# Kernel optimization log

Measured on AMD Instinct MI355X. Metric: run time of the kernel, lower is better.

## Reference

```python
import jax, jax.numpy as jnp
import numpy as np

B, L, D, H = 4, 2048, 1024, 16
HD = D // H  # head_dim = 64


def setup_inputs() -> dict:
    key = jax.random.key(0)
    k1, k2, k3, k4 = jax.random.split(key, 4)
    x = jax.random.normal(k1, (B, L, D), dtype=jnp.float32)
    key_padding_mask = jax.random.randint(k2, (B, L), 0, 2) == 1
    scale = 1.0 / np.sqrt(D)
    Wqkv = jax.random.normal(k3, (3 * D, D), dtype=jnp.float32) * scale
    Wproj = jax.random.normal(k4, (D, D), dtype=jnp.float32) * scale
    return {"x": x, "key_padding_mask": key_padding_mask, "Wqkv": Wqkv, "Wproj": Wproj}


def reference(x, key_padding_mask, Wqkv, Wproj):
    b, l, d = x.shape
    qkv = jnp.einsum('bld,ed->ble', x, Wqkv)          # [B, L, 3D]
    q, k, v = jnp.split(qkv, 3, axis=-1)
    # [B, H, L, HD]
    q = q.reshape(b, l, H, HD).transpose(0, 2, 1, 3)
    k = k.reshape(b, l, H, HD).transpose(0, 2, 1, 3)
    v = v.reshape(b, l, H, HD).transpose(0, 2, 1, 3)
    scale = 1.0 / jnp.sqrt(jnp.asarray(HD, dtype=x.dtype))
    scores = jnp.einsum('bhqd,bhkd->bhqk', q, k) * scale  # [B, H, L, L]
    # key_padding_mask True = PAD -> -inf bias on key axis
    bias = jnp.where(key_padding_mask[:, None, None, :], -jnp.inf, 0.0).astype(x.dtype)
    attn = jax.nn.softmax(scores + bias, axis=-1)
    y = jnp.einsum('bhqk,bhkd->bhqd', attn, v)            # [B, H, L, HD]
    y = y.transpose(0, 2, 1, 3).reshape(b, l, d)          # [B, L, D]
    return jnp.einsum('bld,ed->ble', y, Wproj)
```

## Files before the change

### kernel.cpp

```cpp
#include <hip/hip_runtime.h>

#define L_SEQ 2048
#define DIM   1024
#define NH    16
#define HDIM  64
#define KDIM  1024

typedef short  short8 __attribute__((ext_vector_type(8)));
typedef __bf16 bf16x8 __attribute__((ext_vector_type(8)));
typedef __bf16 bf16x4 __attribute__((ext_vector_type(4)));
typedef float  f32x4  __attribute__((ext_vector_type(4)));
typedef unsigned u32x4 __attribute__((ext_vector_type(4)));

__device__ __forceinline__ unsigned short f2bf(float f) {
  unsigned u = __builtin_bit_cast(unsigned, f);
  u += 0x7fffu + ((u >> 16) & 1u);
  return (unsigned short)(u >> 16);
}

__device__ __forceinline__ void gload16(const void* g, void* l) {
  __builtin_amdgcn_global_load_lds(
      (const __attribute__((address_space(1))) void*)g,
      (__attribute__((address_space(3))) void*)l, 16, 0, 0);
}

__device__ __forceinline__ unsigned cvtpk(float a, float b) {
  unsigned r;
  asm("v_cvt_pk_bf16_f32 %0, %1, %2" : "=v"(r) : "v"(a), "v"(b));
  return r;
}
__device__ __forceinline__ void xchg(unsigned &a, unsigned &b) {
  asm("v_permlane32_swap_b32 %0, %1" : "+v"(a), "+v"(b));
  asm("v_permlane16_swap_b32 %0, %1" : "+v"(a), "+v"(b));
}

__global__ __launch_bounds__(256) void cvt_bf16(const float* __restrict__ src,
                                                unsigned short* __restrict__ dst,
                                                int n) {
  int i = (blockIdx.x * 256 + threadIdx.x) * 8;
  if (i >= n) return;
  f32x4 a = *(const f32x4*)(src + i);
  f32x4 b = *(const f32x4*)(src + i + 4);
  short8 o;
  o[0] = (short)f2bf(a[0]); o[1] = (short)f2bf(a[1]);
  o[2] = (short)f2bf(a[2]); o[3] = (short)f2bf(a[3]);
  o[4] = (short)f2bf(b[0]); o[5] = (short)f2bf(b[1]);
  o[6] = (short)f2bf(b[2]); o[7] = (short)f2bf(b[3]);
  *(short8*)(dst + i) = o;
}

__global__ __launch_bounds__(256) void zero_buf(f32x4* __restrict__ dst, int n4) {
  int i = blockIdx.x * 256 + threadIdx.x;
  if (i < n4) dst[i] = f32x4{0.f, 0.f, 0.f, 0.f};
}

__global__ __launch_bounds__(256) void mask_scan(const int* __restrict__ mask,
                                                 int* __restrict__ idx,
                                                 int* __restrict__ lc) {
  const int b = blockIdx.x, t = threadIdx.x;
  __shared__ int wsum[4];
  const int* mrow = mask + b * L_SEQ + t * 8;
  int m[8], c = 0;
#pragma unroll
  for (int i = 0; i < 8; ++i) { m[i] = mrow[i]; c += (m[i] == 0); }
  const int lane = t & 63, w = t >> 6;
  int sc = c;
#pragma unroll
  for (int d = 1; d < 64; d <<= 1) {
    int v = __shfl_up(sc, d);
    if (lane >= d) sc += v;
  }
  if (lane == 63) wsum[w] = sc;
  __syncthreads();
  int pre = sc - c;
  for (int i = 0; i < w; ++i) pre += wsum[i];
  int run = pre;
#pragma unroll
  for (int i = 0; i < 8; ++i) {
    idx[b * L_SEQ + t * 8 + i] = m[i] ? -1 : run;
    run += (m[i] == 0);
  }
  if (t == 255) lc[b] = run;
}

__device__ __forceinline__ void gemm128_mainloop(
    const unsigned short* __restrict__ A, const unsigned short* __restrict__ Bt,
    int m0, int n0, unsigned short* As, unsigned short* Bs, f32x4 (&acc)[4][4]) {
  const int t = threadIdx.x;
  const int wid = t >> 6, lane = t & 63;
  const int wm = wid >> 1, wn = wid & 1;
  const int lr = lane & 15, lk = (lane >> 4) * 8;
  for (int kt = 0; kt < KDIM / 64; ++kt) {
    __syncthreads();
#pragma unroll
    for (int i = 0; i < 4; ++i) {
      int c = i * 256 + t;
      int row = c >> 3, cc = (c & 7) * 8;
      gload16(A  + (size_t)(m0 + row) * KDIM + kt * 64 + cc, As + c * 8);
      gload16(Bt + (size_t)(n0 + row) * KDIM + kt * 64 + cc, Bs + c * 8);
    }
    asm volatile("s_waitcnt vmcnt(0)" ::: "memory");
    __syncthreads();
    bf16x8 af[4][2], bfv[4][2];
#pragma unroll
    for (int mf = 0; mf < 4; ++mf)
#pragma unroll
      for (int kh = 0; kh < 2; ++kh)
        af[mf][kh] = __builtin_bit_cast(bf16x8,
            *(const short8*)(As + (wm * 64 + mf * 16 + lr) * 64 + kh * 32 + lk));
#pragma unroll
    for (int nf = 0; nf < 4; ++nf)
#pragma unroll
      for (int kh = 0; kh < 2; ++kh)
        bfv[nf][kh] = __builtin_bit_cast(bf16x8,
            *(const short8*)(Bs + (wn * 64 + nf * 16 + lr) * 64 + kh * 32 + lk));
#pragma unroll
    for (int mf = 0; mf < 4; ++mf)
#pragma unroll
      for (int nf = 0; nf < 4; ++nf)
#pragma unroll
        for (int kh = 0; kh < 2; ++kh)
          acc[mf][nf] = __builtin_amdgcn_mfma_f32_16x16x32_bf16(
              af[mf][kh], bfv[nf][kh], acc[mf][nf], 0, 0, 0);
  }
}

__global__ __launch_bounds__(256) void gemm_qkv(
    const unsigned short* __restrict__ xb, const unsigned short* __restrict__ wb,
    const int* __restrict__ idx,
    unsigned short* __restrict__ qw, unsigned short* __restrict__ kw,
    unsigned short* __restrict__ vtw) {
  __shared__ unsigned short As[128 * 64], Bs[128 * 64];
  f32x4 acc[4][4] = {};
  const int n0 = blockIdx.x * 128, m0 = blockIdx.y * 128;
  gemm128_mainloop(xb, wb, m0, n0, As, Bs, acc);
  const int t = threadIdx.x, wid = t >> 6, lane = t & 63;
  const int wm = wid >> 1, wn = wid & 1;
  const int sec = n0 >> 10;
  const int nb = n0 & 1023;
  if (sec == 0) {
#pragma unroll
    for (int mf = 0; mf < 4; ++mf)
#pragma unroll
      for (int nf = 0; nf < 4; ++nf) {
        int e = nb + wn * 64 + nf * 16 + (lane & 15);
        int h = e >> 6, hd = e & 63;
#pragma unroll
        for (int r = 0; r < 4; ++r) {
          int m = m0 + wm * 64 + mf * 16 + (lane >> 4) * 4 + r;
          int b = m >> 11, li = m & 2047;
          qw[(((size_t)(b * NH + h)) * L_SEQ + li) * HDIM + hd] =
              f2bf(acc[mf][nf][r]);
        }
      }
  } else {
#pragma unroll
    for (int mf = 0; mf < 4; ++mf)
#pragma unroll
      for (int r = 0; r < 4; ++r) {
        int m = m0 + wm * 64 + mf * 16 + (lane >> 4) * 4 + r;
        int b = m >> 11, li = m & 2047;
        int tgt = idx[b * L_SEQ + li];
        if (tgt < 0) continue;
        size_t bb = (size_t)b * NH;
#pragma unroll
        for (int nf = 0; nf < 4; ++nf) {
          int e = nb + wn * 64 + nf * 16 + (lane & 15);
          int h = e >> 6, hd = e & 63;
          unsigned short val = f2bf(acc[mf][nf][r]);
          if (sec == 1) kw[((bb + h) * L_SEQ + tgt) * HDIM + hd] = val;
          else          vtw[((bb + h) * HDIM + hd) * L_SEQ + tgt] = val;
        }
      }
  }
}

__global__ __launch_bounds__(256) void gemm_proj(
    const unsigned short* __restrict__ yb, const unsigned short* __restrict__ wb,
    float* __restrict__ out) {
  __shared__ unsigned short As[128 * 64], Bs[128 * 64];
  f32x4 acc[4][4] = {};
  const int n0 = blockIdx.x * 128, m0 = blockIdx.y * 128;
  gemm128_mainloop(yb, wb, m0, n0, As, Bs, acc);
  const int t = threadIdx.x, wid = t >> 6, lane = t & 63;
  const int wm = wid >> 1, wn = wid & 1;
#pragma unroll
  for (int mf = 0; mf < 4; ++mf)
#pragma unroll
    for (int nf = 0; nf < 4; ++nf) {
      int e = n0 + wn * 64 + nf * 16 + (lane & 15);
#pragma unroll
      for (int r = 0; r < 4; ++r) {
        int m = m0 + wm * 64 + mf * 16 + (lane >> 4) * 4 + r;
        out[(size_t)m * DIM + e] = acc[mf][nf][r];
      }
    }
}

__global__ __launch_bounds__(256, 4) void attn_kernel(
    const unsigned short* __restrict__ qw, const unsigned short* __restrict__ kw,
    const unsigned short* __restrict__ vtw, const int* __restrict__ lc,
    unsigned short* __restrict__ yb) {
  __shared__ unsigned short Ks[2][64 * 64];
  __shared__ unsigned short Vts[2][64 * 64];
  const int bh = blockIdx.y;
  const int q0 = blockIdx.x * 128;
  const int b = bh >> 4, h = bh & 15;
  const int t = threadIdx.x, wid = t >> 6, lane = t & 63;
  const int lr = lane & 15, lk = (lane >> 4) * 8, g4 = (lane >> 4) * 4;
  const int swr = (lr & 7) << 3;
  const float KE = 0.18033688011112042f;

  const int Lcv = lc[b];
  const int nt = (Lcv + 63) >> 6;

  bf16x8 qf[2][2];
  const size_t qbase = (size_t)bh * L_SEQ + q0 + wid * 32;
#pragma unroll
  for (int qi = 0; qi < 2; ++qi)
#pragma unroll
    for (int kh = 0; kh < 2; ++kh)
      qf[qi][kh] = __builtin_bit_cast(bf16x8,
          *(const short8*)(qw + (qbase + qi * 16 + lr) * HDIM + kh * 32 + lk));

  f32x4 o[2][4] = {};
  float mrun[2] = {-3.0e38f, -3.0e38f};
  float lrun[2] = {0.f, 0.f};

  auto stage = [&](int buf, int kt) {
#pragma unroll
    for (int i = 0; i < 2; ++i) {
      int c = i * 256 + t;
      int row = c >> 3;
      int cs = ((c & 7) ^ (row & 7)) * 8;
      gload16(kw  + ((size_t)bh * L_SEQ + kt * 64 + row) * HDIM + cs, &Ks[buf][c * 8]);
      gload16(vtw + ((size_t)bh * HDIM + row) * L_SEQ + kt * 64 + cs, &Vts[buf][c * 8]);
    }
  };

  stage(0, 0);
  int cur = 0;

  for (int kt = 0; kt < nt; ++kt) {
    if (kt + 1 < nt) {
      stage(cur ^ 1, kt + 1);
      asm volatile("s_waitcnt vmcnt(4)" ::: "memory");
    } else {
      asm volatile("s_waitcnt vmcnt(0)" ::: "memory");
    }
    __builtin_amdgcn_s_barrier();
    __builtin_amdgcn_sched_barrier(0);

    const unsigned short* Kc = Ks[cur];
    f32x4 s[2][4] = {};
    __builtin_amdgcn_s_setprio(1);
#pragma unroll
    for (int nf = 0; nf < 4; ++nf) {
      bf16x8 k0 = __builtin_bit_cast(bf16x8,
          *(const short8*)(Kc + (nf * 16 + lr) * 64 + ((0 + lk) ^ swr)));
      bf16x8 k1 = __builtin_bit_cast(bf16x8,
          *(const short8*)(Kc + (nf * 16 + lr) * 64 + ((32 + lk) ^ swr)));
      s[0][nf] = __builtin_amdgcn_mfma_f32_16x16x32_bf16(k0, qf[0][0], s[0][nf], 0, 0, 0);
      s[0][nf] = __builtin_amdgcn_mfma_f32_16x16x32_bf16(k1, qf[0][1], s[0][nf], 0, 0, 0);
      s[1][nf] = __builtin_amdgcn_mfma_f32_16x16x32_bf16(k0, qf[1][0], s[1][nf], 0, 0, 0);
      s[1][nf] = __builtin_amdgcn_mfma_f32_16x16x32_bf16(k1, qf[1][1], s[1][nf], 0, 0, 0);
    }
    __builtin_amdgcn_s_setprio(0);

    if (kt == nt - 1) {
      int kbase = kt * 64 + g4;
#pragma unroll
      for (int nf = 0; nf < 4; ++nf)
#pragma unroll
        for (int r = 0; r < 4; ++r)
          if (kbase + nf * 16 + r >= Lcv) {
            s[0][nf][r] = -3.0e38f;
            s[1][nf][r] = -3.0e38f;
          }
    }

    float pmax[2];
#pragma unroll
    for (int qi = 0; qi < 2; ++qi) {
      float a0 = fmaxf(fmaxf(s[qi][0][0], s[qi][0][1]), fmaxf(s[qi][0][2], s[qi][0][3]));
      float a1 = fmaxf(fmaxf(s[qi][1][0], s[qi][1][1]), fmaxf(s[qi][1][2], s[qi][1][3]));
      float a2 = fmaxf(fmaxf(s[qi][2][0], s[qi][2][1]), fmaxf(s[qi][2][2], s[qi][2][3]));
      float a3 = fmaxf(fmaxf(s[qi][3][0], s[qi][3][1]), fmaxf(s[qi][3][2], s[qi][3][3]));
      float mm = fmaxf(fmaxf(a0, a1), fmaxf(a2, a3));
      mm = fmaxf(mm, __shfl_xor(mm, 16));
      mm = fmaxf(mm, __shfl_xor(mm, 32));
      pmax[qi] = mm;
    }

    bool need = (pmax[0] > mrun[0] + 8.0f) || (pmax[1] > mrun[1] + 8.0f);
    if (__any(need)) {
#pragma unroll
      for (int qi = 0; qi < 2; ++qi) {
        float mn = fmaxf(mrun[qi], pmax[qi]);
        float al = __builtin_amdgcn_exp2f((mrun[qi] - mn) * KE);
        mrun[qi] = mn;
        lrun[qi] *= al;
#pragma unroll
        for (int df = 0; df < 4; ++df) o[qi][df] *= al;
      }
    }

    bf16x8 pb[2][2];
#pragma unroll
    for (int qi = 0; qi < 2; ++qi) {
      float mk_ = mrun[qi] * KE;
      f32x4 rs4 = {0.f, 0.f, 0.f, 0.f};
#pragma unroll
      for (int nf = 0; nf < 4; ++nf) {
#pragma unroll
        for (int r = 0; r < 4; ++r)
          s[qi][nf][r] = __builtin_amdgcn_exp2f(s[qi][nf][r] * KE - mk_);
        rs4 += s[qi][nf];
      }
      float rsum = (rs4[0] + rs4[1]) + (rs4[2] + rs4[3]);
      rsum += __shfl_xor(rsum, 16);
      rsum += __shfl_xor(rsum, 32);
      lrun[qi] += rsum;
      unsigned w00 = cvtpk(s[qi][0][0], s[qi][0][1]);
      unsigned w01 = cvtpk(s[qi][0][2], s[qi][0][3]);
      unsigned w10 = cvtpk(s[qi][1][0], s[qi][1][1]);
      unsigned w11 = cvtpk(s[qi][1][2], s[qi][1][3]);
      unsigned w20 = cvtpk(s[qi][2][0], s[qi][2][1]);
      unsigned w21 = cvtpk(s[qi][2][2], s[qi][2][3]);
      unsigned w30 = cvtpk(s[qi][3][0], s[qi][3][1]);
      unsigned w31 = cvtpk(s[qi][3][2], s[qi][3][3]);
      xchg(w00, w10);
      xchg(w01, w11);
      xchg(w20, w30);
      xchg(w21, w31);
      u32x4 f0 = {w00, w01, w10, w11};
      u32x4 f1 = {w20, w21, w30, w31};
      pb[qi][0] = __builtin_bit_cast(bf16x8, f0);
      pb[qi][1] = __builtin_bit_cast(bf16x8, f1);
    }

    const unsigned short* Vc = Vts[cur];
    __builtin_amdgcn_s_setprio(1);
#pragma unroll
    for (int df = 0; df < 4; ++df) {
      bf16x8 v0 = __builtin_bit_cast(bf16x8,
          *(const short8*)(Vc + (df * 16 + lr) * 64 + ((0 + lk) ^ swr)));
      bf16x8 v1 = __builtin_bit_cast(bf16x8,
          *(const short8*)(Vc + (df * 16 + lr) * 64 + ((32 + lk) ^ swr)));
      o[0][df] = __builtin_amdgcn_mfma_f32_16x16x32_bf16(v0, pb[0][0], o[0][df], 0, 0, 0);
      o[0][df] = __builtin_amdgcn_mfma_f32_16x16x32_bf16(v1, pb[0][1], o[0][df], 0, 0, 0);
      o[1][df] = __builtin_amdgcn_mfma_f32_16x16x32_bf16(v0, pb[1][0], o[1][df], 0, 0, 0);
      o[1][df] = __builtin_amdgcn_mfma_f32_16x16x32_bf16(v1, pb[1][1], o[1][df], 0, 0, 0);
    }
    __builtin_amdgcn_s_setprio(0);

    __builtin_amdgcn_sched_barrier(0);
    __builtin_amdgcn_s_barrier();
    cur ^= 1;
  }

#pragma unroll
  for (int qi = 0; qi < 2; ++qi) {
    float inv = 1.0f / lrun[qi];
    int q = q0 + wid * 32 + qi * 16 + lr;
#pragma unroll
    for (int df = 0; df < 4; ++df) {
      bf16x4 pk = {(__bf16)(o[qi][df][0] * inv), (__bf16)(o[qi][df][1] * inv),
                   (__bf16)(o[qi][df][2] * inv), (__bf16)(o[qi][df][3] * inv)};
      *(bf16x4*)(yb + ((size_t)b * L_SEQ + q) * DIM + h * 64 + df * 16 + g4) = pk;
    }
  }
}

extern "C" void kernel_launch(void* const* d_in, const int* in_sizes, int n_in,
                              void* d_out, int out_size, void* d_ws, size_t ws_size,
                              hipStream_t stream) {
  const float* x     = (const float*)d_in[0];
  const int*   mask  = (const int*)d_in[1];
  const float* wqkv  = (const float*)d_in[2];
  const float* wproj = (const float*)d_in[3];
  char* ws = (char*)d_ws;
  unsigned short* xb     = (unsigned short*)(ws + 0);
  unsigned short* wqkvb  = (unsigned short*)(ws + 16777216);
  unsigned short* wprojb = (unsigned short*)(ws + 23068672);
  unsigned short* qw     = (unsigned short*)(ws + 25165824);
  unsigned short* kw     = (unsigned short*)(ws + 41943040);
  unsigned short* vtw    = (unsigned short*)(ws + 58720256);
  unsigned short* yb     = (unsigned short*)(ws + 75497472);
  int*            idx    = (int*)(ws + 92274688);
  int*            lcArr  = (int*)(ws + 92307456);

  cvt_bf16<<<dim3(8388608 / 2048), 256, 0, stream>>>(x, xb, 8388608);
  cvt_bf16<<<dim3(3145728 / 2048), 256, 0, stream>>>(wqkv, wqkvb, 3145728);
  cvt_bf16<<<dim3(1048576 / 2048), 256, 0, stream>>>(wproj, wprojb, 1048576);
  mask_scan<<<dim3(4), 256, 0, stream>>>(mask, idx, lcArr);
  zero_buf<<<dim3(4096), 256, 0, stream>>>((f32x4*)vtw, 1048576);
  gemm_qkv<<<dim3(24, 64), 256, 0, stream>>>(xb, wqkvb, idx, qw, kw, vtw);
  attn_kernel<<<dim3(16, 64), 256, 0, stream>>>(qw, kw, vtw, lcArr, yb);
  gemm_proj<<<dim3(8, 64), 256, 0, stream>>>(yb, wprojb, (float*)d_out);
}
```

Measured before the change: 185.0 us.

## Rewrite GEMM mainloop as 256x128 double-buffered, swizzled, 8-wave pipelined tile

Replaces the single-buffered 128x128 GEMM mainloop used by the QKV and output projections with a 256x128 tile computed by 8 waves. Shared memory is double-buffered, and global-to-LDS loads for the next K step are issued during MFMA work. LDS reads use an XOR swizzle to avoid bank conflicts, and the compute is split into four interleaved phases with priority hints. The aim is to hide global-load latency and raise MFMA utilisation, at the cost of more LDS (96KB per block), fewer blocks, and more barriers per iteration.

```diff
diff --git a/kernel.cpp b/kernel.cpp
--- a/kernel.cpp
+++ b/kernel.cpp
@@ -23,6 +23,11 @@
       (const __attribute__((address_space(1))) void*)g,
       (__attribute__((address_space(3))) void*)l, 16, 0, 0);
 }
+
+__device__ __forceinline__ bf16x8 ldfrag(const unsigned short* p) {
+  return __builtin_bit_cast(bf16x8, *(const short8*)p);
+}
+#define MFMA16(a, b, c) __builtin_amdgcn_mfma_f32_16x16x32_bf16(a, b, c, 0, 0, 0)
 
 __device__ __forceinline__ unsigned cvtpk(float a, float b) {
   unsigned r;
@@ -83,71 +88,145 @@
   if (t == 255) lc[b] = run;
 }
 
-__device__ __forceinline__ void gemm128_mainloop(
+__device__ __forceinline__ void gemm256_mainloop(
     const unsigned short* __restrict__ A, const unsigned short* __restrict__ Bt,
-    int m0, int n0, unsigned short* As, unsigned short* Bs, f32x4 (&acc)[4][4]) {
+    int m0, int n0,
+    unsigned short* As0, unsigned short* As1,
+    unsigned short* Bs0, unsigned short* Bs1,
+    f32x4 (&acc)[8][2]) {
   const int t = threadIdx.x;
-  const int wid = t >> 6, lane = t & 63;
-  const int wm = wid >> 1, wn = wid & 1;
+  const int lane = t & 63, wid = t >> 6;
+  const int wm = wid >> 2, wn = wid & 3;
   const int lr = lane & 15, lk = (lane >> 4) * 8;
-  for (int kt = 0; kt < KDIM / 64; ++kt) {
-    __syncthreads();
-#pragma unroll
-    for (int i = 0; i < 4; ++i) {
-      int c = i * 256 + t;
-      int row = c >> 3, cc = (c & 7) * 8;
-      gload16(A  + (size_t)(m0 + row) * KDIM + kt * 64 + cc, As + c * 8);
-      gload16(Bt + (size_t)(n0 + row) * KDIM + kt * 64 + cc, Bs + c * 8);
-    }
-    asm volatile("s_waitcnt vmcnt(0)" ::: "memory");
-    __syncthreads();
-    bf16x8 af[4][2], bfv[4][2];
+  const int swr = (lr & 7) << 3;
+  constexpr int NT = KDIM / 64;
+
+  auto stageA = [&](unsigned short* dst, int kt, int h) {
+#pragma unroll
+    for (int i = 0; i < 2; ++i) {
+      int c = i * 512 + t;
+      int row = h * 128 + (c >> 3);
+      int cs = ((c & 7) ^ (row & 7)) * 8;
+      gload16(A + (size_t)(m0 + row) * KDIM + kt * 64 + cs,
+              dst + row * 64 + (c & 7) * 8);
+    }
+  };
+  auto stageB = [&](unsigned short* dst, int kt) {
+#pragma unroll
+    for (int i = 0; i < 2; ++i) {
+      int c = i * 512 + t;
+      int row = c >> 3;
+      int cs = ((c & 7) ^ (row & 7)) * 8;
+      gload16(Bt + (size_t)(n0 + row) * KDIM + kt * 64 + cs,
+              dst + row * 64 + (c & 7) * 8);
+    }
+  };
+
+  stageA(As0, 0, 0); stageA(As0, 0, 1); stageB(Bs0, 0);
+  stageA(As1, 1, 0); stageA(As1, 1, 1);
+
+  unsigned short *Ac = As0, *An = As1, *Bc = Bs0, *Bn = Bs1;
+
+  for (int T = 0; T < NT; ++T) {
+    if (T == NT - 1) { asm volatile("s_waitcnt vmcnt(0)" ::: "memory"); }
+    else             { asm volatile("s_waitcnt vmcnt(4)" ::: "memory"); }
+    __builtin_amdgcn_s_barrier();
+    __builtin_amdgcn_sched_barrier(0);
+
+    if (T + 1 < NT) stageB(Bn, T + 1);
+    bf16x8 a[4][2], a2[4][2], b0[2], b1[2];
 #pragma unroll
     for (int mf = 0; mf < 4; ++mf)
 #pragma unroll
       for (int kh = 0; kh < 2; ++kh)
-        af[mf][kh] = __builtin_bit_cast(bf16x8,
-            *(const short8*)(As + (wm * 64 + mf * 16 + lr) * 64 + kh * 32 + lk));
-#pragma unroll
-    for (int nf = 0; nf < 4; ++nf)
+        a[mf][kh] = ldfrag(Ac + (wm * 128 + mf * 16 + lr) * 64 +
+                           ((kh * 32 + lk) ^ swr));
+#pragma unroll
+    for (int kh = 0; kh < 2; ++kh)
+      b0[kh] = ldfrag(Bc + (wn * 32 + lr) * 64 + ((kh * 32 + lk) ^ swr));
+    asm volatile("s_waitcnt lgkmcnt(0)" ::: "memory");
+    __builtin_amdgcn_sched_barrier(0);
+    __builtin_amdgcn_s_setprio(1);
+#pragma unroll
+    for (int mf = 0; mf < 4; ++mf) {
+      acc[mf][0] = MFMA16(a[mf][0], b0[0], acc[mf][0]);
+      acc[mf][0] = MFMA16(a[mf][1], b0[1], acc[mf][0]);
+    }
+    __builtin_amdgcn_s_setprio(0);
+    __builtin_amdgcn_s_barrier();
+
+#pragma unroll
+    for (int kh = 0; kh < 2; ++kh)
+      b1[kh] = ldfrag(Bc + (wn * 32 + 16 + lr) * 64 + ((kh * 32 + lk) ^ swr));
+    asm volatile("s_waitcnt lgkmcnt(0)" ::: "memory");
+    __builtin_amdgcn_sched_barrier(0);
+    __builtin_amdgcn_s_setprio(1);
+#pragma unroll
+    for (int mf = 0; mf < 4; ++mf) {
+      acc[mf][1] = MFMA16(a[mf][0], b1[0], acc[mf][1]);
+      acc[mf][1] = MFMA16(a[mf][1], b1[1], acc[mf][1]);
+    }
+    __builtin_amdgcn_s_setprio(0);
+    __builtin_amdgcn_s_barrier();
+
+#pragma unroll
+    for (int mf = 0; mf < 4; ++mf)
 #pragma unroll
       for (int kh = 0; kh < 2; ++kh)
-        bfv[nf][kh] = __builtin_bit_cast(bf16x8,
-            *(const short8*)(Bs + (wn * 64 + nf * 16 + lr) * 64 + kh * 32 + lk));
-#pragma unroll
-    for (int mf = 0; mf < 4; ++mf)
-#pragma unroll
-      for (int nf = 0; nf < 4; ++nf)
-#pragma unroll
-        for (int kh = 0; kh < 2; ++kh)
-          acc[mf][nf] = __builtin_amdgcn_mfma_f32_16x16x32_bf16(
-              af[mf][kh], bfv[nf][kh], acc[mf][nf], 0, 0, 0);
-  }
-}
-
-__global__ __launch_bounds__(256) void gemm_qkv(
+        a2[mf][kh] = ldfrag(Ac + (wm * 128 + 64 + mf * 16 + lr) * 64 +
+                            ((kh * 32 + lk) ^ swr));
+    asm volatile("s_waitcnt lgkmcnt(0)" ::: "memory");
+    __builtin_amdgcn_sched_barrier(0);
+    __builtin_amdgcn_s_setprio(1);
+#pragma unroll
+    for (int mf = 0; mf < 4; ++mf) {
+      acc[mf + 4][0] = MFMA16(a2[mf][0], b0[0], acc[mf + 4][0]);
+      acc[mf + 4][0] = MFMA16(a2[mf][1], b0[1], acc[mf + 4][0]);
+    }
+    __builtin_amdgcn_s_setprio(0);
+    __builtin_amdgcn_s_barrier();
+    __builtin_amdgcn_sched_barrier(0);
+
+    if (T + 2 < NT) { stageA(Ac, T + 2, 0); stageA(Ac, T + 2, 1); }
+    __builtin_amdgcn_s_setprio(1);
+#pragma unroll
+    for (int mf = 0; mf < 4; ++mf) {
+      acc[mf + 4][1] = MFMA16(a2[mf][0], b1[0], acc[mf + 4][1]);
+      acc[mf + 4][1] = MFMA16(a2[mf][1], b1[1], acc[mf + 4][1]);
+    }
+    __builtin_amdgcn_s_setprio(0);
+
+    unsigned short* tp;
+    tp = Ac; Ac = An; An = tp;
+    tp = Bc; Bc = Bn; Bn = tp;
+  }
+}
+
+__global__ __launch_bounds__(512, 2) void gemm_qkv(
     const unsigned short* __restrict__ xb, const unsigned short* __restrict__ wb,
     const int* __restrict__ idx,
     unsigned short* __restrict__ qw, unsigned short* __restrict__ kw,
     unsigned short* __restrict__ vtw) {
-  __shared__ unsigned short As[128 * 64], Bs[128 * 64];
-  f32x4 acc[4][4] = {};
-  const int n0 = blockIdx.x * 128, m0 = blockIdx.y * 128;
-  gemm128_mainloop(xb, wb, m0, n0, As, Bs, acc);
-  const int t = threadIdx.x, wid = t >> 6, lane = t & 63;
-  const int wm = wid >> 1, wn = wid & 1;
+  __shared__ unsigned short As[2][256 * 64];
+  __shared__ unsigned short Bs[2][128 * 64];
+  f32x4 acc[8][2] = {};
+  const int n0 = blockIdx.x * 128, m0 = blockIdx.y * 256;
+  gemm256_mainloop(xb, wb, m0, n0, As[0], As[1], Bs[0], Bs[1], acc);
+  const int t = threadIdx.x, lane = t & 63, wid = t >> 6;
+  const int wm = wid >> 2, wn = wid & 3;
+  const int lr = lane & 15, g4 = ((lane >> 4) & 3) * 4;
   const int sec = n0 >> 10;
   const int nb = n0 & 1023;
   if (sec == 0) {
 #pragma unroll
-    for (int mf = 0; mf < 4; ++mf)
-#pragma unroll
-      for (int nf = 0; nf < 4; ++nf) {
-        int e = nb + wn * 64 + nf * 16 + (lane & 15);
+    for (int mf = 0; mf < 8; ++mf)
+#pragma unroll
+      for (int nf = 0; nf < 2; ++nf) {
+        int e = nb + wn * 32 + nf * 16 + lr;
         int h = e >> 6, hd = e & 63;
 #pragma unroll
         for (int r = 0; r < 4; ++r) {
-          int m = m0 + wm * 64 + mf * 16 + (lane >> 4) * 4 + r;
+          int m = m0 + wm * 128 + mf * 16 + g4 + r;
           int b = m >> 11, li = m & 2047;
           qw[(((size_t)(b * NH + h)) * L_SEQ + li) * HDIM + hd] =
               f2bf(acc[mf][nf][r]);
@@ -155,17 +234,17 @@
       }
   } else {
 #pragma unroll
-    for (int mf = 0; mf < 4; ++mf)
+    for (int mf = 0; mf < 8; ++mf)
 #pragma unroll
       for (int r = 0; r < 4; ++r) {
-        int m = m0 + wm * 64 + mf * 16 + (lane >> 4) * 4 + r;
+        int m = m0 + wm * 128 + mf * 16 + g4 + r;
         int b = m >> 11, li = m & 2047;
         int tgt = idx[b * L_SEQ + li];
         if (tgt < 0) continue;
         size_t bb = (size_t)b * NH;
 #pragma unroll
-        for (int nf = 0; nf < 4; ++nf) {
-          int e = nb + wn * 64 + nf * 16 + (lane & 15);
+        for (int nf = 0; nf < 2; ++nf) {
+          int e = nb + wn * 32 + nf * 16 + lr;
           int h = e >> 6, hd = e & 63;
           unsigned short val = f2bf(acc[mf][nf][r]);
           if (sec == 1) kw[((bb + h) * L_SEQ + tgt) * HDIM + hd] = val;
@@ -175,23 +254,25 @@
   }
 }
 
-__global__ __launch_bounds__(256) void gemm_proj(
+__global__ __launch_bounds__(512, 2) void gemm_proj(
     const unsigned short* __restrict__ yb, const unsigned short* __restrict__ wb,
     float* __restrict__ out) {
-  __shared__ unsigned short As[128 * 64], Bs[128 * 64];
-  f32x4 acc[4][4] = {};
-  const int n0 = blockIdx.x * 128, m0 = blockIdx.y * 128;
-  gemm128_mainloop(yb, wb, m0, n0, As, Bs, acc);
-  const int t = threadIdx.x, wid = t >> 6, lane = t & 63;
-  const int wm = wid >> 1, wn = wid & 1;
-#pragma unroll
-  for (int mf = 0; mf < 4; ++mf)
-#pragma unroll
-    for (int nf = 0; nf < 4; ++nf) {
-      int e = n0 + wn * 64 + nf * 16 + (lane & 15);
+  __shared__ unsigned short As[2][256 * 64];
+  __shared__ unsigned short Bs[2][128 * 64];
+  f32x4 acc[8][2] = {};
+  const int n0 = blockIdx.x * 128, m0 = blockIdx.y * 256;
+  gemm256_mainloop(yb, wb, m0, n0, As[0], As[1], Bs[0], Bs[1], acc);
+  const int t = threadIdx.x, lane = t & 63, wid = t >> 6;
+  const int wm = wid >> 2, wn = wid & 3;
+  const int lr = lane & 15, g4 = ((lane >> 4) & 3) * 4;
+#pragma unroll
+  for (int mf = 0; mf < 8; ++mf)
+#pragma unroll
+    for (int nf = 0; nf < 2; ++nf) {
+      int e = n0 + wn * 32 + nf * 16 + lr;
 #pragma unroll
       for (int r = 0; r < 4; ++r) {
-        int m = m0 + wm * 64 + mf * 16 + (lane >> 4) * 4 + r;
+        int m = m0 + wm * 128 + mf * 16 + g4 + r;
         out[(size_t)m * DIM + e] = acc[mf][nf][r];
       }
     }
@@ -260,10 +341,10 @@
           *(const short8*)(Kc + (nf * 16 + lr) * 64 + ((0 + lk) ^ swr)));
       bf16x8 k1 = __builtin_bit_cast(bf16x8,
           *(const short8*)(Kc + (nf * 16 + lr) * 64 + ((32 + lk) ^ swr)));
-      s[0][nf] = __builtin_amdgcn_mfma_f32_16x16x32_bf16(k0, qf[0][0], s[0][nf], 0, 0, 0);
-      s[0][nf] = __builtin_amdgcn_mfma_f32_16x16x32_bf16(k1, qf[0][1], s[0][nf], 0, 0, 0);
-      s[1][nf] = __builtin_amdgcn_mfma_f32_16x16x32_bf16(k0, qf[1][0], s[1][nf], 0, 0, 0);
-      s[1][nf] = __builtin_amdgcn_mfma_f32_16x16x32_bf16(k1, qf[1][1], s[1][nf], 0, 0, 0);
+      s[0][nf] = MFMA16(k0, qf[0][0], s[0][nf]);
+      s[0][nf] = MFMA16(k1, qf[0][1], s[0][nf]);
+      s[1][nf] = MFMA16(k0, qf[1][0], s[1][nf]);
+      s[1][nf] = MFMA16(k1, qf[1][1], s[1][nf]);
     }
     __builtin_amdgcn_s_setprio(0);
 
@@ -347,10 +428,10 @@
           *(const short8*)(Vc + (df * 16 + lr) * 64 + ((0 + lk) ^ swr)));
       bf16x8 v1 = __builtin_bit_cast(bf16x8,
           *(const short8*)(Vc + (df * 16 + lr) * 64 + ((32 + lk) ^ swr)));
-      o[0][df] = __builtin_amdgcn_mfma_f32_16x16x32_bf16(v0, pb[0][0], o[0][df], 0, 0, 0);
-      o[0][df] = __builtin_amdgcn_mfma_f32_16x16x32_bf16(v1, pb[0][1], o[0][df], 0, 0, 0);
-      o[1][df] = __builtin_amdgcn_mfma_f32_16x16x32_bf16(v0, pb[1][0], o[1][df], 0, 0, 0);
-      o[1][df] = __builtin_amdgcn_mfma_f32_16x16x32_bf16(v1, pb[1][1], o[1][df], 0, 0, 0);
+      o[0][df] = MFMA16(v0, pb[0][0], o[0][df]);
+      o[0][df] = MFMA16(v1, pb[0][1], o[0][df]);
+      o[1][df] = MFMA16(v0, pb[1][0], o[1][df]);
+      o[1][df] = MFMA16(v1, pb[1][1], o[1][df]);
     }
     __builtin_amdgcn_s_setprio(0);
 
@@ -395,7 +476,7 @@
   cvt_bf16<<<dim3(1048576 / 2048), 256, 0, stream>>>(wproj, wprojb, 1048576);
   mask_scan<<<dim3(4), 256, 0, stream>>>(mask, idx, lcArr);
   zero_buf<<<dim3(4096), 256, 0, stream>>>((f32x4*)vtw, 1048576);
-  gemm_qkv<<<dim3(24, 64), 256, 0, stream>>>(xb, wqkvb, idx, qw, kw, vtw);
+  gemm_qkv<<<dim3(24, 32), 512, 0, stream>>>(xb, wqkvb, idx, qw, kw, vtw);
   attn_kernel<<<dim3(16, 64), 256, 0, stream>>>(qw, kw, vtw, lcArr, yb);
-  gemm_proj<<<dim3(8, 64), 256, 0, stream>>>(yb, wprojb, (float*)d_out);
-}
+  gemm_proj<<<dim3(8, 32), 512, 0, stream>>>(yb, wprojb, (float*)d_out);
+}
```

Result: slower. 204.2 us (+10.4%).
